# Optimization experiments

Hardware: AMD Instinct MI355X
Metric: run time of the kernel (lower is better)

## Reference

```python
import jax, jax.numpy as jnp
import numpy as np

CURV_BOUNDS = (-2.0, 2.0)
THRESH = 0.01   # |k| below this -> Euclidean branch
EPS = 1e-5

B, S, D = 4, 2048, 512


def setup_inputs() -> dict:
    key = jax.random.key(0)
    ks = jax.random.split(key, 8)
    x = jax.random.normal(ks[0], (B, S, D), jnp.float32)
    sc = 1.0 / np.sqrt(D)  # ~ nn.Linear default init scale
    Wq = jax.random.uniform(ks[1], (D, D), jnp.float32, -sc, sc)
    bq = jax.random.uniform(ks[2], (D,), jnp.float32, -sc, sc)
    Wk = jax.random.uniform(ks[3], (D, D), jnp.float32, -sc, sc)
    bk = jax.random.uniform(ks[4], (D,), jnp.float32, -sc, sc)
    Wv = jax.random.uniform(ks[5], (D, D), jnp.float32, -sc, sc)
    bv = jax.random.uniform(ks[6], (D,), jnp.float32, -sc, sc)
    curvature_raw = jnp.float32(0.5)   # init_curvature
    temperature = jnp.float32(1.0)
    mask = jnp.triu(jnp.ones((S, S), dtype=bool), 1)  # causal: True = masked out
    return {"x": x, "Wq": Wq, "bq": bq, "Wk": Wk, "bk": bk, "Wv": Wv,
            "bv": bv, "curvature_raw": curvature_raw,
            "temperature": temperature, "mask": mask}


def _curvature(raw):
    k_min, k_max = CURV_BOUNDS
    return k_min + (k_max - k_min) * (jnp.tanh(raw) + 1.0) / 2.0


def _project(u, k):
    # project_to_manifold: identity (euclid), Poincare-ball clip (k<0), sphere renorm (k>0)
    n = jnp.sqrt(jnp.sum(u * u, axis=-1, keepdims=True) + 1e-12)
    absk = jnp.abs(k)
    sk = jnp.sqrt(jnp.maximum(absk, EPS))
    max_norm = (1.0 - 1e-3) / sk                      # ball radius 1/sqrt(|k|)
    u_hyp = u * jnp.minimum(1.0, max_norm / n)
    u_sph = u / (n * sk)                              # sphere radius 1/sqrt(k)
    return jnp.where(absk < THRESH, u, jnp.where(k < 0, u_hyp, u_sph))


def reference(x, Wq, bq, Wk, bk, Wv, bv, curvature_raw, temperature, mask):
    k = _curvature(curvature_raw)
    q = x @ Wq.T + bq
    kk = x @ Wk.T + bk
    v = x @ Wv.T + bv
    qm = _project(q, k)
    km = _project(kk, k)

    # pairwise quantities without materializing [B,S,S,D]
    dots = jnp.einsum('bid,bjd->bij', qm, km)         # [B,S,S]
    qn2 = jnp.sum(qm * qm, axis=-1)                   # [B,S]
    kn2 = jnp.sum(km * km, axis=-1)                   # [B,S]
    diff2 = jnp.maximum(qn2[:, :, None] + kn2[:, None, :] - 2.0 * dots, 0.0)

    absk = jnp.abs(k)
    sk = jnp.sqrt(jnp.maximum(absk, EPS))

    d_euc = jnp.sqrt(diff2 + 1e-12)
    # hyperbolic (Poincare ball, c=|k|): acosh(1 + 2c|x-y|^2 / ((1-c|x|^2)(1-c|y|^2))) / sqrt(c)
    denom = jnp.maximum((1.0 - absk * qn2)[:, :, None] * (1.0 - absk * kn2)[:, None, :], EPS)
    arg = 1.0 + 2.0 * absk * diff2 / denom
    d_hyp = jnp.arccosh(jnp.maximum(arg, 1.0 + 1e-7)) / sk
    # spherical (radius 1/sqrt(k)): arccos(k * <x,y>) / sqrt(k)
    cosang = jnp.clip(absk * dots, -1.0 + 1e-7, 1.0 - 1e-7)
    d_sph = jnp.arccos(cosang) / sk

    dist = jnp.where(absk < THRESH, d_euc, jnp.where(k < 0, d_hyp, d_sph))

    scores = -dist / (temperature + 1e-8)
    scores = jnp.where(mask[None, :, :], -jnp.inf, scores)
    attention = jax.nn.softmax(scores, axis=-1)       # [B,S,S]
    output = jnp.einsum('bij,bjd->bid', attention, v) # [B,S,D]
    return output, attention
```

## Files before the change

kernel.cpp:

```cpp
#include <hip/hip_runtime.h>
#include <hip/hip_bf16.h>
#include <math.h>

typedef unsigned short u16;
typedef float float4e __attribute__((ext_vector_type(4)));
typedef short short8 __attribute__((ext_vector_type(8)));
typedef unsigned short ushort8 __attribute__((ext_vector_type(8)));

#define SEQ 2048
#define DIM 512
#define NB  4

__device__ __forceinline__ float bf2f(u16 h) {
    return __uint_as_float(((unsigned)h) << 16);
}
__device__ __forceinline__ u16 f2bf(float f) {
    __hip_bfloat16 h = __float2bfloat16(f);
    return *reinterpret_cast<u16*>(&h);
}
__device__ __forceinline__ float curv_of(float raw) {
    return -2.0f + 2.0f * (tanhf(raw) + 1.0f);
}
__device__ __forceinline__ void gl_lds16(const u16* g, u16* lds) {
    __builtin_amdgcn_global_load_lds(
        (const __attribute__((address_space(1))) unsigned int*)g,
        (__attribute__((address_space(3))) unsigned int*)lds, 16, 0, 0);
}

__global__ __launch_bounds__(256) void cvt_all_kernel(
    const float* __restrict__ x, const float* __restrict__ Wq,
    const float* __restrict__ Wk, const float* __restrict__ Wv,
    u16* __restrict__ x_bf, u16* __restrict__ Wcat, float* __restrict__ lsum)
{
    int i = blockIdx.x * 256 + threadIdx.x;
    const int n_x = NB * SEQ * DIM, n_w = DIM * DIM;
    if (i < NB * SEQ) lsum[i] = 0.f;
    if (i < n_x) {
        x_bf[i] = f2bf(x[i]);
    } else if (i < n_x + 3 * n_w) {
        int j = i - n_x;
        const float* W = (j < n_w) ? Wq : (j < 2 * n_w ? Wk : Wv);
        int off = j % n_w;
        Wcat[j] = f2bf(W[off]);
    }
}

template<int MODE>
__global__ __launch_bounds__(256) void gemm64_kernel(
    const u16* __restrict__ A, int lda, long long sA,
    const u16* __restrict__ Bt, int ldb, long long sB,
    void* __restrict__ Cv, int ldc, long long sC,
    float* __restrict__ lsum,
    const float* __restrict__ bq, const float* __restrict__ bk, const float* __restrict__ bv,
    const float* __restrict__ qn2v, const float* __restrict__ kn2v,
    const float* __restrict__ curvp, const float* __restrict__ tempp)
{
    int bn = blockIdx.x, bm = blockIdx.y, b = blockIdx.z;
    int t = threadIdx.x, wave = t >> 6, lane = t & 63;

    if (MODE == 1) {
        if (bn > bm) {
            if (bn == bm + 1 && !(bm & 1)) {
                u16* Cb = (u16*)Cv + (size_t)b * sC;
                int r = t >> 2, seg = t & 3;
                int4 z = {0, 0, 0, 0};
                int4* p = (int4*)&Cb[(size_t)(bm * 64 + r) * ldc + bn * 64 + seg * 16];
                p[0] = z; p[1] = z;
            }
            return;
        }
    }

    __shared__ __align__(16) u16 As[64 * 128];
    __shared__ __align__(16) u16 Bs[64 * 128];

    int wr = wave >> 1, wc = wave & 1;
    int lrow = lane & 15, quad = lane >> 4;
    int rl = lane >> 4, cs = lane & 15;

    const u16* Ab = A + (size_t)b * sA + (size_t)(bm * 64) * lda;
    const u16* Bb = Bt + (size_t)b * sB + (size_t)(bn * 64) * ldb;

    float4e acc[2][2];
#pragma unroll
    for (int i = 0; i < 2; i++)
#pragma unroll
        for (int j = 0; j < 2; j++) acc[i][j] = (float4e){0.f, 0.f, 0.f, 0.f};

    int kIters = (MODE == 2) ? ((bm + 2) >> 1) : 4;

    for (int kt = 0; kt < kIters; ++kt) {
        int k0 = kt << 7;
        __syncthreads();
#pragma unroll
        for (int h = 0; h < 4; ++h) {
            int row = wave * 16 + h * 4 + rl;
            int c = cs ^ (row & 15);
            gl_lds16(Ab + (size_t)row * lda + k0 + c * 8, &As[(wave * 16 + h * 4) * 128]);
            gl_lds16(Bb + (size_t)row * ldb + k0 + c * 8, &Bs[(wave * 16 + h * 4) * 128]);
        }
        __syncthreads();
#pragma unroll
        for (int s = 0; s < 4; ++s) {
            short8 af[2], bfr[2];
#pragma unroll
            for (int im = 0; im < 2; im++) {
                int row = wr * 32 + im * 16 + lrow;
                af[im] = *(const short8*)&As[(row * 16 + ((s * 4 + quad) ^ (row & 15))) * 8];
            }
#pragma unroll
            for (int in = 0; in < 2; in++) {
                int row = wc * 32 + in * 16 + lrow;
                bfr[in] = *(const short8*)&Bs[(row * 16 + ((s * 4 + quad) ^ (row & 15))) * 8];
            }
#pragma unroll
            for (int im = 0; im < 2; im++)
#pragma unroll
                for (int in = 0; in < 2; in++)
                    acc[im][in] = __builtin_amdgcn_mfma_f32_16x16x32_bf16(af[im], bfr[in], acc[im][in], 0, 0, 0);
        }
    }

    if (MODE == 0) {
        u16* Cb = (u16*)Cv;
#pragma unroll
        for (int im = 0; im < 2; im++)
#pragma unroll
            for (int in = 0; in < 2; in++)
#pragma unroll
                for (int r = 0; r < 4; r++) {
                    int gi = bm * 64 + wr * 32 + im * 16 + quad * 4 + r;
                    int gj = bn * 64 + wc * 32 + in * 16 + lrow;
                    float bias = (gj < 512) ? bq[gj] : (gj < 1024 ? bk[gj - 512] : bv[gj - 1024]);
                    Cb[(size_t)gi * ldc + gj] = f2bf(acc[im][in][r] + bias);
                }
    } else if (MODE == 1) {
        float kv = curv_of(curvp[0]);
        float absk = fabsf(kv);
        float sk = sqrtf(fmaxf(absk, 1e-5f));
        float invT = 1.0f / (tempp[0] + 1e-8f);
        u16* Cb = (u16*)Cv + (size_t)b * sC;

        float psum[2][4];
#pragma unroll
        for (int im = 0; im < 2; im++)
#pragma unroll
            for (int r = 0; r < 4; r++) psum[im][r] = 0.f;

#pragma unroll
        for (int im = 0; im < 2; im++) {
#pragma unroll
            for (int r = 0; r < 4; r++) {
                int gi = bm * 64 + wr * 32 + im * 16 + quad * 4 + r;
                float qn = qn2v[b * SEQ + gi];
#pragma unroll
                for (int in = 0; in < 2; in++) {
                    int gj = bn * 64 + wc * 32 + in * 16 + lrow;
                    float kn = kn2v[b * SEQ + gj];
                    float dot = acc[im][in][r];
                    float diff2 = fmaxf(qn + kn - 2.f * dot, 0.f);
                    float dist;
                    if (absk < 0.01f) {
                        dist = sqrtf(diff2 + 1e-12f);
                    } else if (kv < 0.f) {
                        float denom = fmaxf((1.f - absk * qn) * (1.f - absk * kn), 1e-5f);
                        float arg = fmaxf(1.f + 2.f * absk * diff2 / denom, 1.f + 1e-7f);
                        dist = acoshf(arg) / sk;
                    } else {
                        float c = fminf(fmaxf(absk * dot, -1.f + 1e-7f), 1.f - 1e-7f);
                        dist = acosf(c) / sk;
                    }
                    float s = -dist * invT;
                    float e = (gj <= gi) ? __expf(s) : 0.f;
                    Cb[(size_t)gi * ldc + gj] = f2bf(e);
                    psum[im][r] += e;
                }
            }
        }
#pragma unroll
        for (int im = 0; im < 2; im++)
#pragma unroll
            for (int r = 0; r < 4; r++) {
                float v = psum[im][r];
                v += __shfl_xor(v, 1);
                v += __shfl_xor(v, 2);
                v += __shfl_xor(v, 4);
                v += __shfl_xor(v, 8);
                if (lrow == 0) {
                    int gi = bm * 64 + wr * 32 + im * 16 + quad * 4 + r;
                    atomicAdd(&lsum[b * SEQ + gi], v);
                }
            }
    } else {
        float* Cb = (float*)Cv + (size_t)b * sC;
#pragma unroll
        for (int im = 0; im < 2; im++)
#pragma unroll
            for (int r = 0; r < 4; r++) {
                int gi = bm * 64 + wr * 32 + im * 16 + quad * 4 + r;
                float invl = 1.0f / lsum[b * SEQ + gi];
#pragma unroll
                for (int in = 0; in < 2; in++) {
                    int gd = bn * 64 + wc * 32 + in * 16 + lrow;
                    Cb[(size_t)gi * ldc + gd] = acc[im][in][r] * invl;
                }
            }
    }
}

__global__ __launch_bounds__(256) void project_kernel(
    const u16* __restrict__ qkvh,
    u16* __restrict__ qm, u16* __restrict__ km,
    float* __restrict__ qn2, float* __restrict__ kn2,
    const float* __restrict__ curvp)
{
    int r = blockIdx.x;
    int t = threadIdx.x;
    float kv = curv_of(curvp[0]);
    float absk = fabsf(kv);
    float sk = sqrtf(fmaxf(absk, 1e-5f));

    const u16* qrow = qkvh + (size_t)r * 1536;
    const u16* krow = qrow + 512;
    float q0 = bf2f(qrow[t]), q1 = bf2f(qrow[t + 256]);
    float k0 = bf2f(krow[t]), k1 = bf2f(krow[t + 256]);

    float sq = q0 * q0 + q1 * q1;
    float s2 = k0 * k0 + k1 * k1;
#pragma unroll
    for (int off = 32; off > 0; off >>= 1) {
        sq += __shfl_down(sq, off);
        s2 += __shfl_down(s2, off);
    }
    __shared__ float rq[4], rk[4];
    int wave = t >> 6, lane = t & 63;
    if (lane == 0) { rq[wave] = sq; rk[wave] = s2; }
    __syncthreads();
    float n2q = rq[0] + rq[1] + rq[2] + rq[3];
    float n2k = rk[0] + rk[1] + rk[2] + rk[3];

    float sclq, sclk;
    {
        float nq = sqrtf(n2q + 1e-12f);
        float nk = sqrtf(n2k + 1e-12f);
        if (absk < 0.01f) { sclq = 1.f; sclk = 1.f; }
        else if (kv < 0.f) {
            float mx = (1.0f - 1e-3f) / sk;
            sclq = fminf(1.f, mx / nq);
            sclk = fminf(1.f, mx / nk);
        } else {
            sclq = 1.f / (nq * sk);
            sclk = 1.f / (nk * sk);
        }
    }
    if (t == 0) {
        qn2[r] = n2q * sclq * sclq;
        kn2[r] = n2k * sclk * sclk;
    }
    u16* qo = qm + (size_t)r * 512;
    u16* ko = km + (size_t)r * 512;
    qo[t]       = f2bf(q0 * sclq);
    qo[t + 256] = f2bf(q1 * sclq);
    ko[t]       = f2bf(k0 * sclk);
    ko[t + 256] = f2bf(k1 * sclk);
}

__global__ __launch_bounds__(256) void transpose_v_kernel(
    const u16* __restrict__ qkvh, u16* __restrict__ vT)
{
    __shared__ u16 tile[32][33];
    int b = blockIdx.z;
    int s0 = blockIdx.x * 32, d0 = blockIdx.y * 32;
    int tx = threadIdx.x, ty = threadIdx.y;
#pragma unroll
    for (int r = 0; r < 4; r++) {
        int s = s0 + ty + r * 8;
        tile[ty + r * 8][tx] = qkvh[(size_t)(b * SEQ + s) * 1536 + 1024 + d0 + tx];
    }
    __syncthreads();
#pragma unroll
    for (int r = 0; r < 4; r++) {
        int d = d0 + ty + r * 8;
        int s = s0 + tx;
        vT[((size_t)b * DIM + d) * SEQ + s] = tile[tx][ty + r * 8];
    }
}

__global__ __launch_bounds__(256) void norm_attn_kernel(
    const u16* __restrict__ attnH, const float* __restrict__ lsum,
    float* __restrict__ attnF)
{
    int i = blockIdx.x, b = blockIdx.y, t = threadIdx.x;
    float inv = 1.0f / lsum[b * SEQ + i];
    const u16* rowh = attnH + ((size_t)b * SEQ + i) * SEQ;
    float* row = attnF + ((size_t)b * SEQ + i) * SEQ;
    int L = i + 1;
    int j0 = t * 8;
    float4 lo, hi;
    if (j0 + 8 <= L) {
        ushort8 h = *(const ushort8*)&rowh[j0];
        lo.x = bf2f(h[0]) * inv; lo.y = bf2f(h[1]) * inv;
        lo.z = bf2f(h[2]) * inv; lo.w = bf2f(h[3]) * inv;
        hi.x = bf2f(h[4]) * inv; hi.y = bf2f(h[5]) * inv;
        hi.z = bf2f(h[6]) * inv; hi.w = bf2f(h[7]) * inv;
    } else {
        float v[8];
#pragma unroll
        for (int e = 0; e < 8; e++)
            v[e] = (j0 + e < L) ? bf2f(rowh[j0 + e]) * inv : 0.f;
        lo = (float4){v[0], v[1], v[2], v[3]};
        hi = (float4){v[4], v[5], v[6], v[7]};
    }
    *(float4*)&row[j0] = lo;
    *(float4*)&row[j0 + 4] = hi;
}

extern "C" void kernel_launch(void* const* d_in, const int* in_sizes, int n_in,
                              void* d_out, int out_size, void* d_ws, size_t ws_size,
                              hipStream_t stream) {
    (void)in_sizes; (void)n_in; (void)out_size; (void)ws_size;

    const float* x    = (const float*)d_in[0];
    const float* Wq   = (const float*)d_in[1];
    const float* bq   = (const float*)d_in[2];
    const float* Wk   = (const float*)d_in[3];
    const float* bk   = (const float*)d_in[4];
    const float* Wv   = (const float*)d_in[5];
    const float* bv   = (const float*)d_in[6];
    const float* curv = (const float*)d_in[7];
    const float* temp = (const float*)d_in[8];

    float* out   = (float*)d_out;
    float* attnF = out + (size_t)NB * SEQ * DIM;

    char* ws = (char*)d_ws;
    u16*   x_bf  = (u16*)(ws + 0);
    u16*   Wcat  = (u16*)(ws + 8388608);
    u16*   qkvh  = (u16*)(ws + 9961472);
    u16*   qm    = (u16*)(ws + 35127296);
    u16*   km    = (u16*)(ws + 43515904);
    u16*   vT    = (u16*)(ws + 51904512);
    float* qn2   = (float*)(ws + 60293120);
    float* kn2   = (float*)(ws + 60325888);
    float* lsum  = (float*)(ws + 60358656);
    u16*   attnH = (u16*)(ws + 0);

    {
        int n_tot = NB * SEQ * DIM + 3 * DIM * DIM;
        cvt_all_kernel<<<(n_tot + 255) / 256, 256, 0, stream>>>(x, Wq, Wk, Wv, x_bf, Wcat, lsum);
    }

    gemm64_kernel<0><<<dim3(1536 / 64, 8192 / 64, 1), 256, 0, stream>>>(
        x_bf, 512, 0, Wcat, 512, 0, (void*)qkvh, 1536, 0,
        nullptr, bq, bk, bv, nullptr, nullptr, nullptr, nullptr);

    project_kernel<<<NB * SEQ, 256, 0, stream>>>(qkvh, qm, km, qn2, kn2, curv);

    {
        dim3 g(SEQ / 32, DIM / 32, NB), blk(32, 8);
        transpose_v_kernel<<<g, blk, 0, stream>>>(qkvh, vT);
    }

    gemm64_kernel<1><<<dim3(SEQ / 64, SEQ / 64, NB), 256, 0, stream>>>(
        qm, 512, (long long)SEQ * DIM, km, 512, (long long)SEQ * DIM,
        (void*)attnH, SEQ, (long long)SEQ * SEQ,
        lsum, nullptr, nullptr, nullptr, qn2, kn2, curv, temp);

    gemm64_kernel<2><<<dim3(DIM / 64, SEQ / 64, NB), 256, 0, stream>>>(
        attnH, SEQ, (long long)SEQ * SEQ, vT, SEQ, (long long)DIM * SEQ,
        (void*)out, DIM, (long long)SEQ * DIM,
        lsum, nullptr, nullptr, nullptr, nullptr, nullptr, nullptr, nullptr);

    norm_attn_kernel<<<dim3(SEQ, NB), 256, 0, stream>>>(attnH, lsum, attnF);
}
```

Measured before the change: 251.0 us.

## Fuse V transpose into QKV GEMM, split-K PV, vectorize conversion and projection

Several changes land together. The V transpose kernel is removed: the QKV GEMM epilogue writes packed transposed V directly. The K tile shrinks from 128 to 64 with launch bounds requesting more occupancy. The PV GEMM is split two ways over K and accumulates into a zeroed output with float atomics. The conversion kernel is vectorized to float4 and also zeroes the output, and the projection kernel processes one row per wave with 16-byte loads. The zero-fill of the masked diagonal-adjacent tile in the score GEMM is dropped, which relies on the PV loop bounds never reading it; the atomics add traffic and nondeterminism.

```diff
diff --git a/kernel.cpp b/kernel.cpp
--- a/kernel.cpp
+++ b/kernel.cpp
@@ -6,6 +6,7 @@
 typedef float float4e __attribute__((ext_vector_type(4)));
 typedef short short8 __attribute__((ext_vector_type(8)));
 typedef unsigned short ushort8 __attribute__((ext_vector_type(8)));
+typedef unsigned short u16x4 __attribute__((ext_vector_type(4)));
 
 #define SEQ 2048
 #define DIM 512
@@ -30,53 +31,52 @@
 __global__ __launch_bounds__(256) void cvt_all_kernel(
     const float* __restrict__ x, const float* __restrict__ Wq,
     const float* __restrict__ Wk, const float* __restrict__ Wv,
-    u16* __restrict__ x_bf, u16* __restrict__ Wcat, float* __restrict__ lsum)
+    u16* __restrict__ x_bf, u16* __restrict__ Wcat, float* __restrict__ lsum,
+    float* __restrict__ outz)
 {
-    int i = blockIdx.x * 256 + threadIdx.x;
     const int n_x = NB * SEQ * DIM, n_w = DIM * DIM;
-    if (i < NB * SEQ) lsum[i] = 0.f;
-    if (i < n_x) {
-        x_bf[i] = f2bf(x[i]);
-    } else if (i < n_x + 3 * n_w) {
-        int j = i - n_x;
+    const int n_out = NB * SEQ * DIM;
+    int gid = blockIdx.x * 256 + threadIdx.x;
+    if (gid < NB * SEQ) lsum[gid] = 0.f;
+    if (gid < n_out / 4) ((float4*)outz)[gid] = (float4){0.f, 0.f, 0.f, 0.f};
+    int i4 = gid * 4;
+    if (i4 < n_x) {
+        float4 v = *(const float4*)&x[i4];
+        u16x4 h = {f2bf(v.x), f2bf(v.y), f2bf(v.z), f2bf(v.w)};
+        *(u16x4*)&x_bf[i4] = h;
+    } else if (i4 < n_x + 3 * n_w) {
+        int j = i4 - n_x;
         const float* W = (j < n_w) ? Wq : (j < 2 * n_w ? Wk : Wv);
         int off = j % n_w;
-        Wcat[j] = f2bf(W[off]);
+        float4 v = *(const float4*)&W[off];
+        u16x4 h = {f2bf(v.x), f2bf(v.y), f2bf(v.z), f2bf(v.w)};
+        *(u16x4*)&Wcat[j] = h;
     }
 }
 
 template<int MODE>
-__global__ __launch_bounds__(256) void gemm64_kernel(
+__global__ __launch_bounds__(256, 8) void gemm64_kernel(
     const u16* __restrict__ A, int lda, long long sA,
     const u16* __restrict__ Bt, int ldb, long long sB,
     void* __restrict__ Cv, int ldc, long long sC,
+    u16* __restrict__ vT,
     float* __restrict__ lsum,
     const float* __restrict__ bq, const float* __restrict__ bk, const float* __restrict__ bv,
     const float* __restrict__ qn2v, const float* __restrict__ kn2v,
     const float* __restrict__ curvp, const float* __restrict__ tempp)
 {
-    int bn = blockIdx.x, bm = blockIdx.y, b = blockIdx.z;
+    int bx = blockIdx.x, bm = blockIdx.y, b = blockIdx.z;
+    int bn = (MODE == 2) ? (bx & 7) : bx;
+    int kp = (MODE == 2) ? (bx >> 3) : 0;
+    if (MODE == 1 && bn > bm) return;
+
+    __shared__ __align__(16) u16 As[64 * 64];
+    __shared__ __align__(16) u16 Bs[64 * 64];
+
     int t = threadIdx.x, wave = t >> 6, lane = t & 63;
-
-    if (MODE == 1) {
-        if (bn > bm) {
-            if (bn == bm + 1 && !(bm & 1)) {
-                u16* Cb = (u16*)Cv + (size_t)b * sC;
-                int r = t >> 2, seg = t & 3;
-                int4 z = {0, 0, 0, 0};
-                int4* p = (int4*)&Cb[(size_t)(bm * 64 + r) * ldc + bn * 64 + seg * 16];
-                p[0] = z; p[1] = z;
-            }
-            return;
-        }
-    }
-
-    __shared__ __align__(16) u16 As[64 * 128];
-    __shared__ __align__(16) u16 Bs[64 * 128];
-
     int wr = wave >> 1, wc = wave & 1;
     int lrow = lane & 15, quad = lane >> 4;
-    int rl = lane >> 4, cs = lane & 15;
+    int srow = lane >> 3, sc = lane & 7;
 
     const u16* Ab = A + (size_t)b * sA + (size_t)(bm * 64) * lda;
     const u16* Bb = Bt + (size_t)b * sB + (size_t)(bn * 64) * ldb;
@@ -87,31 +87,34 @@
 #pragma unroll
         for (int j = 0; j < 2; j++) acc[i][j] = (float4e){0.f, 0.f, 0.f, 0.f};
 
-    int kIters = (MODE == 2) ? ((bm + 2) >> 1) : 4;
-
-    for (int kt = 0; kt < kIters; ++kt) {
-        int k0 = kt << 7;
+    int ktBeg = (MODE == 2) ? kp : 0;
+    int ktEnd = (MODE == 2) ? (bm + 1) : 8;
+    int ktStp = (MODE == 2) ? 2 : 1;
+
+    for (int kt = ktBeg; kt < ktEnd; kt += ktStp) {
+        int k0 = kt << 6;
         __syncthreads();
 #pragma unroll
-        for (int h = 0; h < 4; ++h) {
-            int row = wave * 16 + h * 4 + rl;
-            int c = cs ^ (row & 15);
-            gl_lds16(Ab + (size_t)row * lda + k0 + c * 8, &As[(wave * 16 + h * 4) * 128]);
-            gl_lds16(Bb + (size_t)row * ldb + k0 + c * 8, &Bs[(wave * 16 + h * 4) * 128]);
+        for (int h = 0; h < 2; ++h) {
+            int q = wave * 2 + h;
+            int row = q * 8 + srow;
+            int c = sc ^ (row & 7);
+            gl_lds16(Ab + (size_t)row * lda + k0 + c * 8, &As[q * 512]);
+            gl_lds16(Bb + (size_t)row * ldb + k0 + c * 8, &Bs[q * 512]);
         }
         __syncthreads();
 #pragma unroll
-        for (int s = 0; s < 4; ++s) {
+        for (int s = 0; s < 2; ++s) {
             short8 af[2], bfr[2];
 #pragma unroll
             for (int im = 0; im < 2; im++) {
-                int row = wr * 32 + im * 16 + lrow;
-                af[im] = *(const short8*)&As[(row * 16 + ((s * 4 + quad) ^ (row & 15))) * 8];
+                int R = wr * 32 + im * 16 + lrow;
+                af[im] = *(const short8*)&As[R * 64 + (((s * 4 + quad) ^ (R & 7)) * 8)];
             }
 #pragma unroll
             for (int in = 0; in < 2; in++) {
-                int row = wc * 32 + in * 16 + lrow;
-                bfr[in] = *(const short8*)&Bs[(row * 16 + ((s * 4 + quad) ^ (row & 15))) * 8];
+                int R = wc * 32 + in * 16 + lrow;
+                bfr[in] = *(const short8*)&Bs[R * 64 + (((s * 4 + quad) ^ (R & 7)) * 8)];
             }
 #pragma unroll
             for (int im = 0; im < 2; im++)
@@ -126,14 +129,22 @@
 #pragma unroll
         for (int im = 0; im < 2; im++)
 #pragma unroll
-            for (int in = 0; in < 2; in++)
+            for (int in = 0; in < 2; in++) {
+                int gi0 = bm * 64 + wr * 32 + im * 16 + quad * 4;
+                int gj = bn * 64 + wc * 32 + in * 16 + lrow;
+                float bias = (gj < 512) ? bq[gj] : (gj < 1024 ? bk[gj - 512] : bv[gj - 1024]);
+                u16x4 pack;
 #pragma unroll
                 for (int r = 0; r < 4; r++) {
-                    int gi = bm * 64 + wr * 32 + im * 16 + quad * 4 + r;
-                    int gj = bn * 64 + wc * 32 + in * 16 + lrow;
-                    float bias = (gj < 512) ? bq[gj] : (gj < 1024 ? bk[gj - 512] : bv[gj - 1024]);
-                    Cb[(size_t)gi * ldc + gj] = f2bf(acc[im][in][r] + bias);
-                }
+                    u16 hv = f2bf(acc[im][in][r] + bias);
+                    Cb[(size_t)(gi0 + r) * ldc + gj] = hv;
+                    pack[r] = hv;
+                }
+                if (gj >= 1024) {
+                    int bb = gi0 >> 11, s = gi0 & 2047;
+                    *(u16x4*)&vT[((size_t)bb * DIM + (gj - 1024)) * SEQ + s] = pack;
+                }
+            }
     } else if (MODE == 1) {
         float kv = curv_of(curvp[0]);
         float absk = fabsf(kv);
@@ -202,7 +213,7 @@
 #pragma unroll
                 for (int in = 0; in < 2; in++) {
                     int gd = bn * 64 + wc * 32 + in * 16 + lrow;
-                    Cb[(size_t)gi * ldc + gd] = acc[im][in][r] * invl;
+                    atomicAdd(&Cb[(size_t)gi * ldc + gd], acc[im][in][r] * invl);
                 }
             }
     }
@@ -214,35 +225,33 @@
     float* __restrict__ qn2, float* __restrict__ kn2,
     const float* __restrict__ curvp)
 {
-    int r = blockIdx.x;
-    int t = threadIdx.x;
+    int wave = threadIdx.x >> 6, lane = threadIdx.x & 63;
+    int r = blockIdx.x * 4 + wave;
     float kv = curv_of(curvp[0]);
     float absk = fabsf(kv);
     float sk = sqrtf(fmaxf(absk, 1e-5f));
 
     const u16* qrow = qkvh + (size_t)r * 1536;
-    const u16* krow = qrow + 512;
-    float q0 = bf2f(qrow[t]), q1 = bf2f(qrow[t + 256]);
-    float k0 = bf2f(krow[t]), k1 = bf2f(krow[t + 256]);
-
-    float sq = q0 * q0 + q1 * q1;
-    float s2 = k0 * k0 + k1 * k1;
-#pragma unroll
-    for (int off = 32; off > 0; off >>= 1) {
-        sq += __shfl_down(sq, off);
-        s2 += __shfl_down(s2, off);
-    }
-    __shared__ float rq[4], rk[4];
-    int wave = t >> 6, lane = t & 63;
-    if (lane == 0) { rq[wave] = sq; rk[wave] = s2; }
-    __syncthreads();
-    float n2q = rq[0] + rq[1] + rq[2] + rq[3];
-    float n2k = rk[0] + rk[1] + rk[2] + rk[3];
+    ushort8 qh = *(const ushort8*)&qrow[lane * 8];
+    ushort8 kh = *(const ushort8*)&qrow[512 + lane * 8];
+
+    float qv[8], kw[8];
+    float sq = 0.f, s2 = 0.f;
+#pragma unroll
+    for (int e = 0; e < 8; e++) {
+        qv[e] = bf2f(qh[e]); sq += qv[e] * qv[e];
+        kw[e] = bf2f(kh[e]); s2 += kw[e] * kw[e];
+    }
+#pragma unroll
+    for (int off = 1; off < 64; off <<= 1) {
+        sq += __shfl_xor(sq, off);
+        s2 += __shfl_xor(s2, off);
+    }
 
     float sclq, sclk;
     {
-        float nq = sqrtf(n2q + 1e-12f);
-        float nk = sqrtf(n2k + 1e-12f);
+        float nq = sqrtf(sq + 1e-12f);
+        float nk = sqrtf(s2 + 1e-12f);
         if (absk < 0.01f) { sclq = 1.f; sclk = 1.f; }
         else if (kv < 0.f) {
             float mx = (1.0f - 1e-3f) / sk;
@@ -253,37 +262,18 @@
             sclk = 1.f / (nk * sk);
         }
     }
-    if (t == 0) {
-        qn2[r] = n2q * sclq * sclq;
-        kn2[r] = n2k * sclk * sclk;
-    }
-    u16* qo = qm + (size_t)r * 512;
-    u16* ko = km + (size_t)r * 512;
-    qo[t]       = f2bf(q0 * sclq);
-    qo[t + 256] = f2bf(q1 * sclq);
-    ko[t]       = f2bf(k0 * sclk);
-    ko[t + 256] = f2bf(k1 * sclk);
-}
-
-__global__ __launch_bounds__(256) void transpose_v_kernel(
-    const u16* __restrict__ qkvh, u16* __restrict__ vT)
-{
-    __shared__ u16 tile[32][33];
-    int b = blockIdx.z;
-    int s0 = blockIdx.x * 32, d0 = blockIdx.y * 32;
-    int tx = threadIdx.x, ty = threadIdx.y;
-#pragma unroll
-    for (int r = 0; r < 4; r++) {
-        int s = s0 + ty + r * 8;
-        tile[ty + r * 8][tx] = qkvh[(size_t)(b * SEQ + s) * 1536 + 1024 + d0 + tx];
-    }
-    __syncthreads();
-#pragma unroll
-    for (int r = 0; r < 4; r++) {
-        int d = d0 + ty + r * 8;
-        int s = s0 + tx;
-        vT[((size_t)b * DIM + d) * SEQ + s] = tile[tx][ty + r * 8];
-    }
+    if (lane == 0) {
+        qn2[r] = sq * sclq * sclq;
+        kn2[r] = s2 * sclk * sclk;
+    }
+    ushort8 qo, ko;
+#pragma unroll
+    for (int e = 0; e < 8; e++) {
+        qo[e] = f2bf(qv[e] * sclq);
+        ko[e] = f2bf(kw[e] * sclk);
+    }
+    *(ushort8*)&qm[(size_t)r * 512 + lane * 8] = qo;
+    *(ushort8*)&km[(size_t)r * 512 + lane * 8] = ko;
 }
 
 __global__ __launch_bounds__(256) void norm_attn_kernel(
@@ -346,30 +336,25 @@
     u16*   attnH = (u16*)(ws + 0);
 
     {
-        int n_tot = NB * SEQ * DIM + 3 * DIM * DIM;
-        cvt_all_kernel<<<(n_tot + 255) / 256, 256, 0, stream>>>(x, Wq, Wk, Wv, x_bf, Wcat, lsum);
+        int n_tot = (NB * SEQ * DIM + 3 * DIM * DIM) / 4;
+        cvt_all_kernel<<<(n_tot + 255) / 256, 256, 0, stream>>>(x, Wq, Wk, Wv, x_bf, Wcat, lsum, out);
     }
 
     gemm64_kernel<0><<<dim3(1536 / 64, 8192 / 64, 1), 256, 0, stream>>>(
         x_bf, 512, 0, Wcat, 512, 0, (void*)qkvh, 1536, 0,
-        nullptr, bq, bk, bv, nullptr, nullptr, nullptr, nullptr);
-
-    project_kernel<<<NB * SEQ, 256, 0, stream>>>(qkvh, qm, km, qn2, kn2, curv);
-
-    {
-        dim3 g(SEQ / 32, DIM / 32, NB), blk(32, 8);
-        transpose_v_kernel<<<g, blk, 0, stream>>>(qkvh, vT);
-    }
+        vT, nullptr, bq, bk, bv, nullptr, nullptr, nullptr, nullptr);
+
+    project_kernel<<<NB * SEQ / 4, 256, 0, stream>>>(qkvh, qm, km, qn2, kn2, curv);
 
     gemm64_kernel<1><<<dim3(SEQ / 64, SEQ / 64, NB), 256, 0, stream>>>(
         qm, 512, (long long)SEQ * DIM, km, 512, (long long)SEQ * DIM,
         (void*)attnH, SEQ, (long long)SEQ * SEQ,
-        lsum, nullptr, nullptr, nullptr, qn2, kn2, curv, temp);
-
-    gemm64_kernel<2><<<dim3(DIM / 64, SEQ / 64, NB), 256, 0, stream>>>(
+        nullptr, lsum, nullptr, nullptr, nullptr, qn2, kn2, curv, temp);
+
+    gemm64_kernel<2><<<dim3(2 * DIM / 64, SEQ / 64, NB), 256, 0, stream>>>(
         attnH, SEQ, (long long)SEQ * SEQ, vT, SEQ, (long long)DIM * SEQ,
         (void*)out, DIM, (long long)SEQ * DIM,
-        lsum, nullptr, nullptr, nullptr, nullptr, nullptr, nullptr, nullptr);
+        nullptr, lsum, nullptr, nullptr, nullptr, nullptr, nullptr, nullptr, nullptr);
 
     norm_attn_kernel<<<dim3(SEQ, NB), 256, 0, stream>>>(attnH, lsum, attnF);
 }
```

Result: faster. 239.4 us (-4.6%).
